# Kernel tuning notes

Hardware: AMD Instinct MI355X
Metric: run time of the kernel (lower is better)

The kernel has to match this reference:

```python
import jax, jax.numpy as jnp
import numpy as np
import math

OMEGA_0 = 30.0
LAYER_SIZES = [3, 256, 256, 256, 256, 3]
N_POINTS = 524288


def _siren_params(key):
    """SIREN initialization matching the original module."""
    keys = jax.random.split(key, len(LAYER_SIZES) - 1)
    params = {}
    for i in range(len(LAYER_SIZES) - 1):
        in_dim, out_dim = LAYER_SIZES[i], LAYER_SIZES[i + 1]
        k = keys[i]
        bound = (1.0 / in_dim) if i == 0 else (math.sqrt(6.0 / in_dim) / OMEGA_0)
        W = jax.random.uniform(k, (out_dim, in_dim), minval=-bound, maxval=bound, dtype=jnp.float32)
        b = jax.random.uniform(k, (out_dim,), minval=-1e-6, maxval=1e-6, dtype=jnp.float32)
        params[f"W{i}"] = W
        params[f"b{i}"] = b
    return params


def setup_inputs() -> dict:
    key = jax.random.key(0)
    kx, kp = jax.random.split(key)
    # coordinates in [-1, 1], typical SIREN input domain
    x = jax.random.uniform(kx, (N_POINTS, 3), minval=-1.0, maxval=1.0, dtype=jnp.float32)
    inp = {"x": x}
    inp.update(_siren_params(kp))
    return inp


def reference(x, W0, b0, W1, b1, W2, b2, W3, b3, W4, b4):
    # First layer: sin(omega_0 * (W0 @ x + b0)), batched over rows of x.
    h = jnp.sin(OMEGA_0 * (jnp.einsum("ni,oi->no", x, W0) + b0))
    # Hidden layers: sin(W @ h + b)
    h = jnp.sin(jnp.einsum("ni,oi->no", h, W1) + b1)
    h = jnp.sin(jnp.einsum("ni,oi->no", h, W2) + b2)
    h = jnp.sin(jnp.einsum("ni,oi->no", h, W3) + b3)
    # Final layer: linear, no activation.
    out = jnp.einsum("ni,oi->no", h, W4) + b4
    return out
```

## Files before the change

kernel.cpp:

```cpp
#include <hip/hip_runtime.h>
#include <stdint.h>


#define OMEGA 30.0f

typedef float    f32x4 __attribute__((ext_vector_type(4)));
typedef short    s16x8 __attribute__((ext_vector_type(8)));
typedef uint32_t u32x4 __attribute__((ext_vector_type(4)));

__device__ __forceinline__ float bf16_to_f32(uint16_t u) {
    uint32_t b = ((uint32_t)u) << 16;
    return __builtin_bit_cast(float, b);
}
__device__ __forceinline__ uint16_t f32_to_bf16(float f) {
    uint32_t u = __builtin_bit_cast(uint32_t, f);
    u += 0x7FFFu + ((u >> 16) & 1u);
    return (uint16_t)(u >> 16);
}
__device__ __forceinline__ uint32_t pack_bf16x2(float lo, float hi) {
    return (uint32_t)f32_to_bf16(lo) | ((uint32_t)f32_to_bf16(hi) << 16);
}

__global__ void convert_weights(const float* __restrict__ W1,
                                const float* __restrict__ W2,
                                const float* __restrict__ W3,
                                uint16_t* __restrict__ wsb) {
    int tid = blockIdx.x * blockDim.x + threadIdx.x;
    int l = tid >> 16;
    int r = tid & 65535;
    int c = r >> 8;
    int k = r & 255;
    const float* W = (l == 0) ? W1 : (l == 1) ? W2 : W3;
    int kc = k >> 5, q = (k >> 3) & 3, j = k & 7;
    wsb[(((l * 8 + kc) * 16 + (c >> 4)) * 64 + q * 16 + (c & 15)) * 8 + j] =
        f32_to_bf16(W[c * 256 + k]);
}

__global__ __launch_bounds__(256, 2) void siren_main(
    const float* __restrict__ x,
    const float* __restrict__ W0, const float* __restrict__ b0,
    const float* __restrict__ b1, const float* __restrict__ b2,
    const float* __restrict__ b3,
    const float* __restrict__ W4, const float* __restrict__ b4,
    const uint16_t* __restrict__ Wb,
    float* __restrict__ out)
{
    __shared__ uint16_t h_lds[2048 * 8];

    const int tid  = threadIdx.x;
    const int lane = tid & 63;
    const int wid  = tid >> 6;
    const int n16  = lane & 15;
    const int q    = lane >> 4;
    const int p0   = blockIdx.x * 64;

    {
        float xv[4][3];
        #pragma unroll
        for (int rt = 0; rt < 4; ++rt) {
            const float* xp = x + (p0 + rt * 16 + n16) * 3;
            xv[rt][0] = xp[0]; xv[rt][1] = xp[1]; xv[rt][2] = xp[2];
        }
        #pragma unroll
        for (int oo = 0; oo < 2; ++oo) {
            const int octet = wid * 8 + oo * 4 + q;
            const float* w0r = W0 + octet * 24;
            float wv[24];
            #pragma unroll
            for (int i = 0; i < 24; ++i) wv[i] = w0r[i];
            float bb[8];
            #pragma unroll
            for (int i = 0; i < 8; ++i) bb[i] = b0[octet * 8 + i];
            const int kc0 = octet >> 2, q0 = octet & 3;
            #pragma unroll
            for (int rt = 0; rt < 4; ++rt) {
                u32x4 pk;
                #pragma unroll
                for (int j2 = 0; j2 < 4; ++j2) {
                    float za = OMEGA * (wv[(2*j2  )*3+0] * xv[rt][0] +
                                        wv[(2*j2  )*3+1] * xv[rt][1] +
                                        wv[(2*j2  )*3+2] * xv[rt][2] + bb[2*j2]);
                    float zb = OMEGA * (wv[(2*j2+1)*3+0] * xv[rt][0] +
                                        wv[(2*j2+1)*3+1] * xv[rt][1] +
                                        wv[(2*j2+1)*3+2] * xv[rt][2] + bb[2*j2+1]);
                    pk[j2] = pack_bf16x2(__sinf(za), __sinf(zb));
                }
                *(u32x4*)&h_lds[((kc0 * 4 + rt) * 64 + q0 * 16 + n16) * 8] = pk;
            }
        }
    }
    __syncthreads();

    #pragma unroll
    for (int l = 0; l < 3; ++l) {
        const uint16_t* wsl = Wb + l * 65536;

        s16x8 Wbuf[2][2][4];
        #pragma unroll
        for (int kc2 = 0; kc2 < 2; ++kc2)
            #pragma unroll
            for (int t = 0; t < 4; ++t)
                Wbuf[0][kc2][t] = *(const s16x8*)(wsl + ((kc2 * 16 + wid * 4 + t) * 64 + lane) * 8);

        f32x4 acc[4][4] = {};
        #pragma unroll
        for (int kp = 0; kp < 4; ++kp) {
            const int cur = kp & 1, nxt = cur ^ 1;
            if (kp < 3) {
                #pragma unroll
                for (int kc2 = 0; kc2 < 2; ++kc2)
                    #pragma unroll
                    for (int t = 0; t < 4; ++t)
                        Wbuf[nxt][kc2][t] = *(const s16x8*)(wsl +
                            (((kp * 2 + 2 + kc2) * 16 + wid * 4 + t) * 64 + lane) * 8);
            }
            #pragma unroll
            for (int kc2 = 0; kc2 < 2; ++kc2) {
                const int kc = kp * 2 + kc2;
                s16x8 hf[4];
                #pragma unroll
                for (int pt = 0; pt < 4; ++pt)
                    hf[pt] = *(const s16x8*)&h_lds[((kc * 4 + pt) * 64 + lane) * 8];
                #pragma unroll
                for (int t = 0; t < 4; ++t)
                    #pragma unroll
                    for (int pt = 0; pt < 4; ++pt)
                        acc[t][pt] = __builtin_amdgcn_mfma_f32_16x16x32_bf16(
                            Wbuf[cur][kc2][t], hf[pt], acc[t][pt], 0, 0, 0);
            }
        }
        __syncthreads();

        const float* bl = (l == 0) ? b1 : (l == 1) ? b2 : b3;
        uint32_t* hw = (uint32_t*)h_lds;
        #pragma unroll
        for (int t = 0; t < 4; ++t) {
            f32x4 bv = *(const f32x4*)&bl[wid * 64 + t * 16 + q * 4];
            const int kcp = wid * 2 + (t >> 1);
            const int qp  = (t * 2 + (q >> 1)) & 3;
            #pragma unroll
            for (int pt = 0; pt < 4; ++pt) {
                float s0 = __sinf(acc[t][pt][0] + bv[0]);
                float s1 = __sinf(acc[t][pt][1] + bv[1]);
                float s2 = __sinf(acc[t][pt][2] + bv[2]);
                float s3 = __sinf(acc[t][pt][3] + bv[3]);
                int base = ((kcp * 4 + pt) * 64 + qp * 16 + n16) * 4 + (q & 1) * 2;
                hw[base + 0] = pack_bf16x2(s0, s1);
                hw[base + 1] = pack_bf16x2(s2, s3);
            }
        }
        __syncthreads();
    }

    if (tid < 192) {
        const int p  = tid & 63;
        const int o  = __builtin_amdgcn_readfirstlane(tid >> 6);
        const int rt = p >> 4, nn = p & 15;
        const float* w4 = W4 + o * 256;
        float sum = b4[o];
        for (int kc = 0; kc < 8; ++kc) {
            #pragma unroll
            for (int qq = 0; qq < 4; ++qq) {
                s16x8 hv = *(const s16x8*)&h_lds[((kc * 4 + rt) * 64 + qq * 16 + nn) * 8];
                #pragma unroll
                for (int e = 0; e < 8; ++e)
                    sum += bf16_to_f32((uint16_t)hv[e]) * w4[kc * 32 + qq * 8 + e];
            }
        }
        out[(p0 + p) * 3 + o] = sum;
    }
}

extern "C" void kernel_launch(void* const* d_in, const int* in_sizes, int n_in,
                              void* d_out, int out_size, void* d_ws, size_t ws_size,
                              hipStream_t stream) {
    const float* x  = (const float*)d_in[0];
    const float* W0 = (const float*)d_in[1];
    const float* b0 = (const float*)d_in[2];
    const float* W1 = (const float*)d_in[3];
    const float* b1 = (const float*)d_in[4];
    const float* W2 = (const float*)d_in[5];
    const float* b2 = (const float*)d_in[6];
    const float* W3 = (const float*)d_in[7];
    const float* b3 = (const float*)d_in[8];
    const float* W4 = (const float*)d_in[9];
    const float* b4 = (const float*)d_in[10];
    float* outp     = (float*)d_out;
    uint16_t* wsb   = (uint16_t*)d_ws;

    hipLaunchKernelGGL(convert_weights, dim3(768), dim3(256), 0, stream,
                       W1, W2, W3, wsb);
    hipLaunchKernelGGL(siren_main, dim3(8192), dim3(256), 0, stream,
                       x, W0, b0, b1, b2, b3, W4, b4, wsb, outp);
}
```

Before: 346.0 us.

## Pre-scale weights by 1/2π for native sin, use MFMA for final layer

New measurement: 328.7 us. -5.0%, faster.

```diff
diff --git a/kernel.cpp b/kernel.cpp
--- a/kernel.cpp
+++ b/kernel.cpp
@@ -2,38 +2,58 @@
 #include <stdint.h>
 
 
-#define OMEGA 30.0f
-
 typedef float    f32x4 __attribute__((ext_vector_type(4)));
 typedef short    s16x8 __attribute__((ext_vector_type(8)));
+typedef uint32_t u32x2 __attribute__((ext_vector_type(2)));
 typedef uint32_t u32x4 __attribute__((ext_vector_type(4)));
 
-__device__ __forceinline__ float bf16_to_f32(uint16_t u) {
-    uint32_t b = ((uint32_t)u) << 16;
-    return __builtin_bit_cast(float, b);
-}
+#define INV2PI 0.15915494309189535f
+#define L0SCALE 4.774648292756860f
+#define W4OFF 196608
+
 __device__ __forceinline__ uint16_t f32_to_bf16(float f) {
     uint32_t u = __builtin_bit_cast(uint32_t, f);
     u += 0x7FFFu + ((u >> 16) & 1u);
     return (uint16_t)(u >> 16);
 }
 __device__ __forceinline__ uint32_t pack_bf16x2(float lo, float hi) {
-    return (uint32_t)f32_to_bf16(lo) | ((uint32_t)f32_to_bf16(hi) << 16);
+#if __has_builtin(__builtin_amdgcn_cvt_pk_bf16_f32)
+    auto v = __builtin_amdgcn_cvt_pk_bf16_f32(lo, hi);
+    return __builtin_bit_cast(uint32_t, v);
+#else
+    uint32_t a = __builtin_bit_cast(uint32_t, lo);
+    uint32_t b = __builtin_bit_cast(uint32_t, hi);
+    a += 0x7FFFu + ((a >> 16) & 1u);
+    b += 0x7FFFu + ((b >> 16) & 1u);
+    return (a >> 16) | (b & 0xFFFF0000u);
+#endif
+}
+__device__ __forceinline__ float sin_rev(float r) {
+    return __builtin_amdgcn_sinf(r);
 }
 
 __global__ void convert_weights(const float* __restrict__ W1,
                                 const float* __restrict__ W2,
                                 const float* __restrict__ W3,
+                                const float* __restrict__ W4,
                                 uint16_t* __restrict__ wsb) {
     int tid = blockIdx.x * blockDim.x + threadIdx.x;
-    int l = tid >> 16;
-    int r = tid & 65535;
-    int c = r >> 8;
-    int k = r & 255;
-    const float* W = (l == 0) ? W1 : (l == 1) ? W2 : W3;
-    int kc = k >> 5, q = (k >> 3) & 3, j = k & 7;
-    wsb[(((l * 8 + kc) * 16 + (c >> 4)) * 64 + q * 16 + (c & 15)) * 8 + j] =
-        f32_to_bf16(W[c * 256 + k]);
+    if (tid < 196608) {
+        int l = tid >> 16;
+        int r = tid & 65535;
+        int c = r >> 8;
+        int k = r & 255;
+        const float* W = (l == 0) ? W1 : (l == 1) ? W2 : W3;
+        int kc = k >> 5, q = (k >> 3) & 3, j = k & 7;
+        wsb[(((l * 8 + kc) * 16 + (c >> 4)) * 64 + q * 16 + (c & 15)) * 8 + j] =
+            f32_to_bf16(W[c * 256 + k] * INV2PI);
+    } else if (tid < 200704) {
+        int e = tid - 196608;
+        int kc = e >> 9, lane = (e >> 3) & 63, j = e & 7;
+        int n16 = lane & 15, q = lane >> 4;
+        float v = (n16 < 3) ? W4[n16 * 256 + kc * 32 + q * 8 + j] : 0.0f;
+        wsb[W4OFF + (kc * 64 + lane) * 8 + j] = f32_to_bf16(v);
+    }
 }
 
 __global__ __launch_bounds__(256, 2) void siren_main(
@@ -41,7 +61,7 @@
     const float* __restrict__ W0, const float* __restrict__ b0,
     const float* __restrict__ b1, const float* __restrict__ b2,
     const float* __restrict__ b3,
-    const float* __restrict__ W4, const float* __restrict__ b4,
+    const float* __restrict__ b4,
     const uint16_t* __restrict__ Wb,
     float* __restrict__ out)
 {
@@ -54,6 +74,11 @@
     const int q    = lane >> 4;
     const int p0   = blockIdx.x * 64;
 
+    s16x8 W4f[8];
+    #pragma unroll
+    for (int kc = 0; kc < 8; ++kc)
+        W4f[kc] = *(const s16x8*)(Wb + W4OFF + (kc * 64 + lane) * 8);
+
     {
         float xv[4][3];
         #pragma unroll
@@ -67,23 +92,23 @@
             const float* w0r = W0 + octet * 24;
             float wv[24];
             #pragma unroll
-            for (int i = 0; i < 24; ++i) wv[i] = w0r[i];
+            for (int i = 0; i < 24; ++i) wv[i] = w0r[i] * L0SCALE;
             float bb[8];
             #pragma unroll
-            for (int i = 0; i < 8; ++i) bb[i] = b0[octet * 8 + i];
+            for (int i = 0; i < 8; ++i) bb[i] = b0[octet * 8 + i] * L0SCALE;
             const int kc0 = octet >> 2, q0 = octet & 3;
             #pragma unroll
             for (int rt = 0; rt < 4; ++rt) {
                 u32x4 pk;
                 #pragma unroll
                 for (int j2 = 0; j2 < 4; ++j2) {
-                    float za = OMEGA * (wv[(2*j2  )*3+0] * xv[rt][0] +
-                                        wv[(2*j2  )*3+1] * xv[rt][1] +
-                                        wv[(2*j2  )*3+2] * xv[rt][2] + bb[2*j2]);
-                    float zb = OMEGA * (wv[(2*j2+1)*3+0] * xv[rt][0] +
-                                        wv[(2*j2+1)*3+1] * xv[rt][1] +
-                                        wv[(2*j2+1)*3+2] * xv[rt][2] + bb[2*j2+1]);
-                    pk[j2] = pack_bf16x2(__sinf(za), __sinf(zb));
+                    float za = wv[(2*j2  )*3+0] * xv[rt][0] +
+                               wv[(2*j2  )*3+1] * xv[rt][1] +
+                               wv[(2*j2  )*3+2] * xv[rt][2] + bb[2*j2];
+                    float zb = wv[(2*j2+1)*3+0] * xv[rt][0] +
+                               wv[(2*j2+1)*3+1] * xv[rt][1] +
+                               wv[(2*j2+1)*3+2] * xv[rt][2] + bb[2*j2+1];
+                    pk[j2] = pack_bf16x2(sin_rev(za), sin_rev(zb));
                 }
                 *(u32x4*)&h_lds[((kc0 * 4 + rt) * 64 + q0 * 16 + n16) * 8] = pk;
             }
@@ -136,38 +161,36 @@
         #pragma unroll
         for (int t = 0; t < 4; ++t) {
             f32x4 bv = *(const f32x4*)&bl[wid * 64 + t * 16 + q * 4];
+            bv *= INV2PI;
             const int kcp = wid * 2 + (t >> 1);
             const int qp  = (t * 2 + (q >> 1)) & 3;
             #pragma unroll
             for (int pt = 0; pt < 4; ++pt) {
-                float s0 = __sinf(acc[t][pt][0] + bv[0]);
-                float s1 = __sinf(acc[t][pt][1] + bv[1]);
-                float s2 = __sinf(acc[t][pt][2] + bv[2]);
-                float s3 = __sinf(acc[t][pt][3] + bv[3]);
+                float s0 = sin_rev(acc[t][pt][0] + bv[0]);
+                float s1 = sin_rev(acc[t][pt][1] + bv[1]);
+                float s2 = sin_rev(acc[t][pt][2] + bv[2]);
+                float s3 = sin_rev(acc[t][pt][3] + bv[3]);
                 int base = ((kcp * 4 + pt) * 64 + qp * 16 + n16) * 4 + (q & 1) * 2;
-                hw[base + 0] = pack_bf16x2(s0, s1);
-                hw[base + 1] = pack_bf16x2(s2, s3);
+                u32x2 w2 = { pack_bf16x2(s0, s1), pack_bf16x2(s2, s3) };
+                *(u32x2*)&hw[base] = w2;
             }
         }
         __syncthreads();
     }
 
-    if (tid < 192) {
-        const int p  = tid & 63;
-        const int o  = __builtin_amdgcn_readfirstlane(tid >> 6);
-        const int rt = p >> 4, nn = p & 15;
-        const float* w4 = W4 + o * 256;
-        float sum = b4[o];
+    {
+        f32x4 accF = {};
+        #pragma unroll
         for (int kc = 0; kc < 8; ++kc) {
-            #pragma unroll
-            for (int qq = 0; qq < 4; ++qq) {
-                s16x8 hv = *(const s16x8*)&h_lds[((kc * 4 + rt) * 64 + qq * 16 + nn) * 8];
-                #pragma unroll
-                for (int e = 0; e < 8; ++e)
-                    sum += bf16_to_f32((uint16_t)hv[e]) * w4[kc * 32 + qq * 8 + e];
-            }
-        }
-        out[(p0 + p) * 3 + o] = sum;
+            s16x8 af = *(const s16x8*)&h_lds[((kc * 4 + wid) * 64 + lane) * 8];
+            accF = __builtin_amdgcn_mfma_f32_16x16x32_bf16(af, W4f[kc], accF, 0, 0, 0);
+        }
+        if (n16 < 3) {
+            float bb4 = b4[n16];
+            #pragma unroll
+            for (int r = 0; r < 4; ++r)
+                out[(p0 + wid * 16 + q * 4 + r) * 3 + n16] = accF[r] + bb4;
+        }
     }
 }
 
@@ -188,8 +211,8 @@
     float* outp     = (float*)d_out;
     uint16_t* wsb   = (uint16_t*)d_ws;
 
-    hipLaunchKernelGGL(convert_weights, dim3(768), dim3(256), 0, stream,
-                       W1, W2, W3, wsb);
+    hipLaunchKernelGGL(convert_weights, dim3(784), dim3(256), 0, stream,
+                       W1, W2, W3, W4, wsb);
     hipLaunchKernelGGL(siren_main, dim3(8192), dim3(256), 0, stream,
-                       x, W0, b0, b1, b2, b3, W4, b4, wsb, outp);
-}
+                       x, W0, b0, b1, b2, b3, b4, wsb, outp);
+}
```
